# Kernel tuning notes

Measured on AMD Instinct MI355X. Metric: run time of the kernel, lower is better.

The kernel has to match this reference:

```python
import jax, jax.numpy as jnp
import numpy as np

B, N, DIM = 64, 197, 768
H = 12
IN_DIM = 768
HD = IN_DIM // H  # 64


def setup_inputs() -> dict:
    key = jax.random.key(0)
    k1, k2, k3 = jax.random.split(key, 3)
    x = jax.random.normal(k1, (B, N, DIM), dtype=jnp.float32)
    # learnable per-head scale, initialized to head_dim**-0.5
    scale = (DIM // H) ** (-0.5) * jnp.ones((H,), dtype=jnp.float32)
    w_qkv = jax.random.normal(k2, (3 * IN_DIM, DIM), dtype=jnp.float32) * 0.02  # qkv_bias=False
    w_proj = jax.random.normal(k3, (IN_DIM, IN_DIM), dtype=jnp.float32) * 0.02
    b_proj = jnp.zeros((IN_DIM,), dtype=jnp.float32)
    return {"x": x, "scale": scale, "w_qkv": w_qkv, "w_proj": w_proj, "b_proj": b_proj}


def reference(x, scale, w_qkv, w_proj, b_proj):
    Bx, Nx, C = x.shape
    # qkv projection -> [3, B, H, N, HD]
    qkv = jnp.einsum('bnc,oc->bno', x, w_qkv).reshape(Bx, Nx, 3, H, HD)
    qkv = qkv.transpose(2, 0, 3, 1, 4)
    q, k, v = qkv[0], qkv[1], qkv[2]
    # per-head learnable scale (LMSA)
    attn = jnp.einsum('bhid,bhjd->bhij', q, k) * scale[None, :, None, None]
    # diagonal mask -> -inf (self-token masking)
    diag = jnp.eye(Nx, dtype=bool)  # [N, N]
    attn = jnp.where(diag[None, None, :, :], -jnp.inf, attn)
    attn = jax.nn.softmax(attn, axis=-1)
    out = jnp.einsum('bhij,bhjd->bhid', attn, v)  # [B, H, N, HD]
    out = out.transpose(0, 2, 1, 3).reshape(Bx, Nx, IN_DIM)
    out = out @ w_proj.T + b_proj
    return out + x  # num_heads > 1 branch: residual add
```

## Files before the change

kernel.cpp:

```cpp
#include <hip/hip_runtime.h>
#include <cstdint>
#include <cstddef>

#define DEV static __device__ __forceinline__

typedef __attribute__((ext_vector_type(8))) short bf16x8;
typedef __attribute__((ext_vector_type(4))) float f32x4;

constexpr int NB   = 64;
constexpr int NTOK = 197;
constexpr int DIMC = 768;
constexpr int NH   = 12;
constexpr int HDIM = 64;
constexpr int MTOK = NB * NTOK;
constexpr int QKVO = 3 * DIMC;
constexpr int BH   = NB * NH;
constexpr int KROWS = 198;
constexpr int VTS   = 232;
constexpr int OBS   = 68;
constexpr int GM64  = MTOK / 64;

constexpr int BM2  = 256;
constexpr int BN2  = 256;
constexpr int GM2  = (MTOK + BM2 - 1) / BM2;
constexpr int GN2  = QKVO / BN2;
constexpr int NKT  = DIMC / 64;
constexpr int BUFH = 32768;

DEV unsigned short f2bf(float f) {
  union { float f; uint32_t u; } v; v.f = f;
  uint32_t u = v.u;
  return (unsigned short)((u + 0x7FFFu + ((u >> 16) & 1u)) >> 16);
}

DEV uint32_t pack_bf2(float a, float b) {
  return (uint32_t)f2bf(a) | ((uint32_t)f2bf(b) << 16);
}

DEV f32x4 mfma16(bf16x8 a, bf16x8 b, f32x4 c) {
  return __builtin_amdgcn_mfma_f32_16x16x32_bf16(a, b, c, 0, 0, 0);
}

DEV void async_cp16(const unsigned short* g, unsigned short* l) {
  __builtin_amdgcn_global_load_lds(
      (__attribute__((address_space(1))) void*)g,
      (__attribute__((address_space(3))) void*)l, 16, 0, 0);
}

DEV void swizzle_idx(int lin, int gridM, int gridN, int& mt, int& nt) {
  int per = 16 * gridN;
  int sup = lin / per;
  int bm  = sup * 16;
  int Gm  = gridM - bm; if (Gm > 16) Gm = 16;
  int rem = lin - sup * per;
  nt = rem / Gm;
  mt = bm + (rem - nt * Gm);
}

constexpr int CVB1 = (MTOK * DIMC) / 4096;
constexpr int CVB2 = (QKVO * DIMC) / 4096;
constexpr int CVB3 = (DIMC * DIMC) / 4096;
constexpr int CVNB = CVB1 + CVB2 + CVB3;

__global__ void __launch_bounds__(256) cvt_all(const float* __restrict__ x,
                                               const float* __restrict__ wq,
                                               const float* __restrict__ wp,
                                               unsigned short* __restrict__ xb,
                                               unsigned short* __restrict__ wqb,
                                               unsigned short* __restrict__ wpb) {
  int blk = blockIdx.x;
  const float* s; unsigned short* d;
  if (blk < CVB1)               { s = x;  d = xb; }
  else if (blk < CVB1 + CVB2)   { s = wq; d = wqb; blk -= CVB1; }
  else                          { s = wp; d = wpb; blk -= CVB1 + CVB2; }
  size_t base = (size_t)blk * 4096 + (size_t)threadIdx.x * 4;
#pragma unroll
  for (int j = 0; j < 4; ++j) {
    size_t i = base + (size_t)j * 1024;
    float4 f = *(const float4*)(s + i);
    ushort4 o;
    o.x = f2bf(f.x); o.y = f2bf(f.y); o.z = f2bf(f.z); o.w = f2bf(f.w);
    *(ushort4*)(d + i) = o;
  }
}

DEV void stage_A_qm(const unsigned short* A, unsigned short* lds,
                    int mbase, int k0, int qm, int tid) {
#pragma unroll
  for (int u = 0; u < 2; ++u) {
    int c = u * 512 + tid;
    int row = c >> 3, cc = c & 7;
    int arow = qm * 64 + (row & 63) + ((row >> 6) << 7);
    int gr = mbase + arow; gr = gr < MTOK ? gr : MTOK - 1;
    int gc = (cc ^ (arow & 7)) * 8;
    async_cp16(A + (size_t)gr * DIMC + k0 + gc, lds + arow * 64 + cc * 8);
  }
}

DEV void stage_B_qn(const unsigned short* Bw, unsigned short* lds,
                    int nbase, int k0, int qn, int tid) {
#pragma unroll
  for (int u = 0; u < 2; ++u) {
    int c = u * 512 + tid;
    int row = c >> 3, cc = c & 7;
    int brow = (row >> 5) * 64 + qn * 32 + (row & 31);
    int gc = (cc ^ (brow & 7)) * 8;
    async_cp16(Bw + (size_t)(nbase + brow) * DIMC + k0 + gc, lds + brow * 64 + cc * 8);
  }
}

template <int QM>
DEV void ldA(const unsigned short* Ac, int wm, int l16, int quad, bf16x8 (&af)[4][2]) {
#pragma unroll
  for (int mi = 0; mi < 4; ++mi)
#pragma unroll
    for (int kk = 0; kk < 2; ++kk) {
      int r = wm * 128 + QM * 64 + mi * 16 + l16;
      af[mi][kk] = *(const bf16x8*)(Ac + r * 64 + (((kk * 4 + quad) ^ (r & 7)) * 8));
    }
}

template <int QN>
DEV void ldB(const unsigned short* Bc, int wn, int l16, int quad, bf16x8 (&bf_)[2][2]) {
#pragma unroll
  for (int ni = 0; ni < 2; ++ni)
#pragma unroll
    for (int kk = 0; kk < 2; ++kk) {
      int r = wn * 64 + QN * 32 + ni * 16 + l16;
      bf_[ni][kk] = *(const bf16x8*)(Bc + r * 64 + (((kk * 4 + quad) ^ (r & 7)) * 8));
    }
}

template <int QM, int QN>
DEV void ph_mfma(bf16x8 (&af)[4][2], bf16x8 (&bf_)[2][2], f32x4 (&acc)[8][4]) {
  __builtin_amdgcn_s_setprio(1);
#pragma unroll
  for (int kk = 0; kk < 2; ++kk)
#pragma unroll
    for (int mi = 0; mi < 4; ++mi)
#pragma unroll
      for (int ni = 0; ni < 2; ++ni)
        acc[QM * 4 + mi][QN * 2 + ni] =
            mfma16(af[mi][kk], bf_[ni][kk], acc[QM * 4 + mi][QN * 2 + ni]);
  __builtin_amdgcn_s_setprio(0);
}

__global__ void __launch_bounds__(512, 2) gemm_qkv(const unsigned short* __restrict__ A,
                                                   const unsigned short* __restrict__ Bw,
                                                   unsigned short* __restrict__ qkv) {
  extern __shared__ unsigned short lds[];
  const int tid = threadIdx.x, lane = tid & 63, wave = tid >> 6;
  const int wm = wave & 1, wn = wave >> 1;
  const int l16 = lane & 15, quad = lane >> 4;
  int mt, nt;
  swizzle_idx(blockIdx.x, GM2, GN2, mt, nt);
  const int mbase = mt * BM2, nbase = nt * BN2;

  f32x4 acc[8][4];
#pragma unroll
  for (int i = 0; i < 8; ++i)
#pragma unroll
    for (int j = 0; j < 4; ++j) acc[i][j] = {0.f, 0.f, 0.f, 0.f};

  unsigned short* A0 = lds;
  unsigned short* B0 = lds + 16384;
  unsigned short* A1 = lds + BUFH;
  unsigned short* B1 = lds + BUFH + 16384;

  stage_A_qm(A, A0, mbase, 0, 0, tid);
  stage_B_qn(Bw, B0, nbase, 0, 0, tid);
  stage_A_qm(A, A0, mbase, 0, 1, tid);
  stage_B_qn(Bw, B0, nbase, 0, 1, tid);
  stage_A_qm(A, A1, mbase, 64, 0, tid);
  stage_B_qn(Bw, B1, nbase, 64, 0, tid);
  asm volatile("s_waitcnt vmcnt(4)" ::: "memory");
  __builtin_amdgcn_s_barrier();

  bf16x8 af[4][2], b0[2][2], b1[2][2];

  for (int kt = 0; kt < NKT; ++kt) {
    unsigned short* Ac = (kt & 1) ? A1 : A0;
    unsigned short* Bc = (kt & 1) ? B1 : B0;
    unsigned short* An = (kt & 1) ? A0 : A1;
    unsigned short* Bn = (kt & 1) ? B0 : B1;

    ldA<0>(Ac, wm, l16, quad, af);
    ldB<0>(Bc, wn, l16, quad, b0);
    if (kt < NKT - 1) stage_A_qm(A, An, mbase, (kt + 1) * 64, 1, tid);
    __builtin_amdgcn_s_barrier();
    ph_mfma<0, 0>(af, b0, acc);
    asm volatile("s_waitcnt lgkmcnt(0)" ::: "memory");
    __builtin_amdgcn_s_barrier();

    ldB<1>(Bc, wn, l16, quad, b1);
    if (kt < NKT - 1) stage_B_qn(Bw, Bn, nbase, (kt + 1) * 64, 1, tid);
    __builtin_amdgcn_s_barrier();
    ph_mfma<0, 1>(af, b1, acc);
    asm volatile("s_waitcnt lgkmcnt(0)" ::: "memory");
    __builtin_amdgcn_s_barrier();

    ldA<1>(Ac, wm, l16, quad, af);
    if (kt < NKT - 2) stage_A_qm(A, Ac, mbase, (kt + 2) * 64, 0, tid);
    __builtin_amdgcn_s_barrier();
    ph_mfma<1, 0>(af, b0, acc);
    asm volatile("s_waitcnt lgkmcnt(0)" ::: "memory");
    __builtin_amdgcn_s_barrier();

    if (kt < NKT - 2) stage_B_qn(Bw, Bc, nbase, (kt + 2) * 64, 0, tid);
    __builtin_amdgcn_s_barrier();
    ph_mfma<1, 1>(af, b1, acc);
    if (kt >= NKT - 2) asm volatile("s_waitcnt vmcnt(0) lgkmcnt(0)" ::: "memory");
    else               asm volatile("s_waitcnt vmcnt(4) lgkmcnt(0)" ::: "memory");
    __builtin_amdgcn_s_barrier();
  }

  const int oc64  = nbase + wn * 64;
  const int which = oc64 / DIMC;
  const int h     = (oc64 % DIMC) / HDIM;
#pragma unroll
  for (int mi8 = 0; mi8 < 8; ++mi8) {
    int t0 = mbase + wm * 128 + mi8 * 16 + quad * 4;
#pragma unroll
    for (int r = 0; r < 4; ++r) {
      int t = t0 + r;
      if (t < MTOK) {
        int b = t / NTOK, n = t - b * NTOK;
        size_t base = ((size_t)((which * NB + b) * NH + h) * NTOK + n) * HDIM;
#pragma unroll
        for (int ni = 0; ni < 4; ++ni)
          qkv[base + ni * 16 + l16] = f2bf(acc[mi8][ni][r]);
      }
    }
  }
}

__global__ void __launch_bounds__(256) gemm_proj(const unsigned short* __restrict__ A,
                                                 const unsigned short* __restrict__ Bw,
                                                 const float* __restrict__ bias,
                                                 const float* __restrict__ xres,
                                                 float* __restrict__ out) {
  __shared__ __align__(16) unsigned short As[64 * 64];
  __shared__ __align__(16) unsigned short Bs[128 * 64];
  const int tid = threadIdx.x, lane = tid & 63, wave = tid >> 6;
  const int wm = wave & 1, wn = wave >> 1;
  const int l16 = lane & 15, quad = lane >> 4;
  int mt, nt;
  swizzle_idx(blockIdx.x, GM64, DIMC / 128, mt, nt);
  const int mbase = mt * 64, nbase = nt * 128;

  f32x4 acc[2][4];
#pragma unroll
  for (int i = 0; i < 2; ++i)
#pragma unroll
    for (int j = 0; j < 4; ++j) acc[i][j] = {0.f, 0.f, 0.f, 0.f};

  for (int k0 = 0; k0 < DIMC; k0 += 64) {
#pragma unroll
    for (int i = 0; i < 2; ++i) {
      int c = i * 256 + tid;
      int row = c >> 3, cc = c & 7;
      int gc = (cc ^ (row & 7)) * 8;
      async_cp16(A + (size_t)(mbase + row) * DIMC + k0 + gc, As + c * 8);
    }
#pragma unroll
    for (int i = 0; i < 4; ++i) {
      int c = i * 256 + tid;
      int row = c >> 3, cc = c & 7;
      int gc = (cc ^ (row & 7)) * 8;
      async_cp16(Bw + (size_t)(nbase + row) * DIMC + k0 + gc, Bs + c * 8);
    }
    __syncthreads();
#pragma unroll
    for (int kk = 0; kk < 64; kk += 32) {
      const int cw = (kk >> 3) + quad;
      bf16x8 af[2], bfr[4];
#pragma unroll
      for (int mi = 0; mi < 2; ++mi) {
        int r = wm * 32 + mi * 16 + l16;
        af[mi] = *(const bf16x8*)(As + r * 64 + (cw ^ (r & 7)) * 8);
      }
#pragma unroll
      for (int ni = 0; ni < 4; ++ni) {
        int r = wn * 64 + ni * 16 + l16;
        bfr[ni] = *(const bf16x8*)(Bs + r * 64 + (cw ^ (r & 7)) * 8);
      }
#pragma unroll
      for (int mi = 0; mi < 2; ++mi)
#pragma unroll
        for (int ni = 0; ni < 4; ++ni)
          acc[mi][ni] = mfma16(af[mi], bfr[ni], acc[mi][ni]);
    }
    __syncthreads();
  }

  const int oc = nbase + wn * 64;
#pragma unroll
  for (int mi = 0; mi < 2; ++mi) {
    int t0 = mbase + wm * 32 + mi * 16 + quad * 4;
#pragma unroll
    for (int r = 0; r < 4; ++r) {
      int t = t0 + r;
      size_t rowb = (size_t)t * DIMC;
#pragma unroll
      for (int ni = 0; ni < 4; ++ni) {
        int o = oc + ni * 16 + l16;
        out[rowb + o] = acc[mi][ni][r] + bias[o] + xres[rowb + o];
      }
    }
  }
}

__global__ void __launch_bounds__(256, 2) attn_fused(const unsigned short* __restrict__ qkv,
                                                     const float* __restrict__ scale,
                                                     unsigned short* __restrict__ aout) {
  __shared__ __align__(16) unsigned short Ks[KROWS * 64];
  __shared__ __align__(16) unsigned short Vt[HDIM * VTS];
  __shared__ __align__(16) unsigned short Ob[4 * 16 * OBS];

  const int tid = threadIdx.x, lane = tid & 63, wave = tid >> 6;
  const int l16 = lane & 15, quad = lane >> 4;
  const int bh = blockIdx.x;
  const int b = bh / NH, h = bh - b * NH;

  const unsigned short* qg = qkv + (size_t)bh * (NTOK * HDIM);
  const unsigned short* kg = qkv + (size_t)(BH + bh) * (NTOK * HDIM);
  const unsigned short* vg = qkv + (size_t)(2 * BH + bh) * (NTOK * HDIM);
  const float sc = scale[h];

#pragma unroll
  for (int i = 0; i < 7; ++i) {
    int c = i * 256 + tid;
    if (c < KROWS * 8) {
      int row = c >> 3, cc = c & 7;
      async_cp16(kg + (size_t)row * 64 + ((cc ^ (row & 7)) * 8), Ks + c * 8);
    }
  }
  {
    const int dcol = tid & 63;
    const int slab = tid >> 6;
#pragma unroll
    for (int p = 0; p < 7; ++p) {
      int n0 = p * 32 + slab * 8;
      union { unsigned short us[8]; bf16x8 v; } tr;
#pragma unroll
      for (int i = 0; i < 8; ++i) {
        int n = n0 + i; n = n > NTOK - 1 ? NTOK - 1 : n;
        tr.us[i] = vg[(size_t)n * HDIM + dcol];
      }
      *(bf16x8*)(Vt + dcol * VTS + n0) = tr.v;
    }
  }
  __syncthreads();

  const int srcA  = l16 + ((quad & 1) << 5);
  const int srcB  = srcA + 16;
  const int stsel = quad >> 1;
  unsigned short* ob = Ob + wave * (16 * OBS);

  for (int mt = wave; mt < 13; mt += 4) {
    int qr = mt * 16 + l16; if (qr > NTOK - 1) qr = NTOK - 1;
    bf16x8 qb0 = *(const bf16x8*)(qg + (size_t)qr * 64 + quad * 8);
    bf16x8 qb1 = *(const bf16x8*)(qg + (size_t)qr * 64 + 32 + quad * 8);
    const int mg = mt * 16 + l16;

    f32x4 s[7][2];
#pragma unroll
    for (int jc = 0; jc < 7; ++jc)
#pragma unroll
      for (int st = 0; st < 2; ++st) {
        if (jc == 6 && st == 1) { s[6][1] = {0.f, 0.f, 0.f, 0.f}; continue; }
        int jrow = (jc * 2 + st) * 16 + l16;
        jrow = jrow > NTOK ? NTOK : jrow;
        const unsigned short* kr = Ks + jrow * 64;
        bf16x8 ka0 = *(const bf16x8*)(kr + (quad       ^ (jrow & 7)) * 8);
        bf16x8 ka1 = *(const bf16x8*)(kr + ((4 + quad) ^ (jrow & 7)) * 8);
        f32x4 t = {0.f, 0.f, 0.f, 0.f};
        t = mfma16(ka0, qb0, t);
        t = mfma16(ka1, qb1, t);
        s[jc][st] = t;
      }

    float cmax = -1e30f;
#pragma unroll
    for (int jc = 0; jc < 7; ++jc)
#pragma unroll
      for (int st = 0; st < 2; ++st)
#pragma unroll
        for (int r = 0; r < 4; ++r) {
          int jg = jc * 32 + st * 16 + quad * 4 + r;
          float v = s[jc][st][r] * sc;
          v = (jg >= NTOK || jg == mg) ? -1e30f : v;
          s[jc][st][r] = v;
          cmax = fmaxf(cmax, v);
        }
    cmax = fmaxf(cmax, __shfl_xor(cmax, 16));
    cmax = fmaxf(cmax, __shfl_xor(cmax, 32));
    float psum = 0.f;
#pragma unroll
    for (int jc = 0; jc < 7; ++jc)
#pragma unroll
      for (int st = 0; st < 2; ++st)
#pragma unroll
        for (int r = 0; r < 4; ++r) {
          float e = __expf(s[jc][st][r] - cmax);
          psum += e;
          s[jc][st][r] = e;
        }
    psum += __shfl_xor(psum, 16);
    psum += __shfl_xor(psum, 32);
    const float inv = 1.0f / psum;

    f32x4 oacc[4];
#pragma unroll
    for (int dt = 0; dt < 4; ++dt) oacc[dt] = {0.f, 0.f, 0.f, 0.f};

#pragma unroll
    for (int jc = 0; jc < 7; ++jc) {
      uint32_t u0 = pack_bf2(s[jc][0][0], s[jc][0][1]);
      uint32_t v0 = pack_bf2(s[jc][0][2], s[jc][0][3]);
      uint32_t u1 = pack_bf2(s[jc][1][0], s[jc][1][1]);
      uint32_t v1 = pack_bf2(s[jc][1][2], s[jc][1][3]);
      uint32_t au0 = (uint32_t)__shfl((int)u0, srcA);
      uint32_t av0 = (uint32_t)__shfl((int)v0, srcA);
      uint32_t au1 = (uint32_t)__shfl((int)u1, srcA);
      uint32_t av1 = (uint32_t)__shfl((int)v1, srcA);
      uint32_t bu0 = (uint32_t)__shfl((int)u0, srcB);
      uint32_t bv0 = (uint32_t)__shfl((int)v0, srcB);
      uint32_t bu1 = (uint32_t)__shfl((int)u1, srcB);
      uint32_t bv1 = (uint32_t)__shfl((int)v1, srcB);
      union { uint32_t u[4]; bf16x8 v; } pb;
      pb.u[0] = stsel ? au1 : au0;
      pb.u[1] = stsel ? av1 : av0;
      pb.u[2] = stsel ? bu1 : bu0;
      pb.u[3] = stsel ? bv1 : bv0;
#pragma unroll
      for (int dt = 0; dt < 4; ++dt) {
        bf16x8 va = *(const bf16x8*)(Vt + (dt * 16 + l16) * VTS +
                                     jc * 32 + quad * 8);
        oacc[dt] = mfma16(va, pb.v, oacc[dt]);
      }
    }

#pragma unroll
    for (int dt = 0; dt < 4; ++dt) {
      ushort4 pk;
      pk.x = f2bf(oacc[dt][0] * inv);
      pk.y = f2bf(oacc[dt][1] * inv);
      pk.z = f2bf(oacc[dt][2] * inv);
      pk.w = f2bf(oacc[dt][3] * inv);
      *(ushort4*)(ob + l16 * OBS + dt * 16 + quad * 4) = pk;
    }
    __asm__ __volatile__("s_waitcnt lgkmcnt(0)" ::: "memory");
#pragma unroll
    for (int rnd = 0; rnd < 4; ++rnd) {
      int q   = rnd * 4 + (lane >> 4);
      int o8  = lane & 15;
      uint2 d8 = *(const uint2*)(ob + q * OBS + o8 * 4);
      int qrow = mt * 16 + q;
      if (qrow < NTOK) {
        size_t obase = (size_t)(b * NTOK + qrow) * DIMC + h * HDIM;
        *(uint2*)(aout + obase + o8 * 4) = d8;
      }
    }
  }
}

extern "C" void kernel_launch(void* const* d_in, const int* in_sizes, int n_in,
                              void* d_out, int out_size, void* d_ws, size_t ws_size,
                              hipStream_t stream) {
  const float* x     = (const float*)d_in[0];
  const float* scale = (const float*)d_in[1];
  const float* wqkv  = (const float*)d_in[2];
  const float* wproj = (const float*)d_in[3];
  const float* bproj = (const float*)d_in[4];
  float* out = (float*)d_out;

  unsigned short* xb   = (unsigned short*)d_ws;
  unsigned short* wqb  = xb  + (size_t)MTOK * DIMC;
  unsigned short* wpb  = wqb + (size_t)QKVO * DIMC;
  unsigned short* qkvb = wpb + (size_t)DIMC * DIMC;
  unsigned short* attb = xb;

  static bool qkv_attr_set = false;
  if (!qkv_attr_set) {
    hipFuncSetAttribute(reinterpret_cast<const void*>(gemm_qkv),
                        hipFuncAttributeMaxDynamicSharedMemorySize, 131072);
    qkv_attr_set = true;
  }

  cvt_all<<<CVNB, 256, 0, stream>>>(x, wqkv, wproj, xb, wqb, wpb);
  gemm_qkv<<<GM2 * GN2, 512, 131072, stream>>>(xb, wqb, qkvb);
  attn_fused<<<BH, 256, 0, stream>>>(qkvb, scale, attb);
  gemm_proj<<<GM64 * (DIMC / 128), 256, 0, stream>>>(attb, wpb, bproj, x, out);
}
```

Measured before the change: 211.2 us.

## Process two QKV GEMM tiles per block and overlap the first tile's epilogue

The QKV GEMM kernel now launches half as many blocks, and each block computes two output tiles back to back in one continuous double-buffered K pipeline. The epilogue is split into four quadrant stores. The first tile's quadrants are written and their accumulators zeroed right after each MFMA phase at the tile boundary, while loads for the second tile are already in flight. The aim is to hide the first tile's global stores and the prologue fill of the second tile behind ongoing work. In exchange, the grid of 225 blocks may leave some CUs idle, and the hand-tuned vmcnt thresholds must exactly match the new load ordering.

```diff
diff --git a/kernel.cpp b/kernel.cpp
--- a/kernel.cpp
+++ b/kernel.cpp
@@ -25,6 +25,8 @@
 constexpr int GM2  = (MTOK + BM2 - 1) / BM2;
 constexpr int GN2  = QKVO / BN2;
 constexpr int NKT  = DIMC / 64;
+constexpr int TOT  = 2 * NKT;
+constexpr int GRID_QKV = (GM2 * GN2) / 2;
 constexpr int BUFH = 32768;
 
 DEV unsigned short f2bf(float f) {
@@ -145,6 +147,34 @@
   __builtin_amdgcn_s_setprio(0);
 }
 
+template <int QM, int QN>
+DEV void epi_quad(f32x4 (&acc)[8][4], unsigned short* __restrict__ qkv,
+                  int mbase, int nbase, int wm, int wn, int l16, int quad) {
+  const int oc32  = nbase + wn * 64 + QN * 32;
+  const int which = oc32 / DIMC;
+  const int h     = (oc32 % DIMC) / HDIM;
+#pragma unroll
+  for (int mi = 0; mi < 4; ++mi) {
+    int t0 = mbase + wm * 128 + QM * 64 + mi * 16 + quad * 4;
+#pragma unroll
+    for (int r = 0; r < 4; ++r) {
+      int t = t0 + r;
+      if (t < MTOK) {
+        int b = t / NTOK, n = t - b * NTOK;
+        size_t base = ((size_t)((which * NB + b) * NH + h) * NTOK + n) * HDIM;
+#pragma unroll
+        for (int ni = 0; ni < 2; ++ni)
+          qkv[base + QN * 32 + ni * 16 + l16] = f2bf(acc[QM * 4 + mi][QN * 2 + ni][r]);
+      }
+    }
+  }
+#pragma unroll
+  for (int mi = 0; mi < 4; ++mi)
+#pragma unroll
+    for (int ni = 0; ni < 2; ++ni)
+      acc[QM * 4 + mi][QN * 2 + ni] = {0.f, 0.f, 0.f, 0.f};
+}
+
 __global__ void __launch_bounds__(512, 2) gemm_qkv(const unsigned short* __restrict__ A,
                                                    const unsigned short* __restrict__ Bw,
                                                    unsigned short* __restrict__ qkv) {
@@ -152,9 +182,15 @@
   const int tid = threadIdx.x, lane = tid & 63, wave = tid >> 6;
   const int wm = wave & 1, wn = wave >> 1;
   const int l16 = lane & 15, quad = lane >> 4;
-  int mt, nt;
-  swizzle_idx(blockIdx.x, GM2, GN2, mt, nt);
-  const int mbase = mt * BM2, nbase = nt * BN2;
+
+  int mbs[2], nbs[2];
+  {
+    int mt, nt;
+    swizzle_idx(blockIdx.x * 2,     GM2, GN2, mt, nt);
+    mbs[0] = mt * BM2; nbs[0] = nt * BN2;
+    swizzle_idx(blockIdx.x * 2 + 1, GM2, GN2, mt, nt);
+    mbs[1] = mt * BM2; nbs[1] = nt * BN2;
+  }
 
   f32x4 acc[8][4];
 #pragma unroll
@@ -167,71 +203,75 @@
   unsigned short* A1 = lds + BUFH;
   unsigned short* B1 = lds + BUFH + 16384;
 
-  stage_A_qm(A, A0, mbase, 0, 0, tid);
-  stage_B_qn(Bw, B0, nbase, 0, 0, tid);
-  stage_A_qm(A, A0, mbase, 0, 1, tid);
-  stage_B_qn(Bw, B0, nbase, 0, 1, tid);
-  stage_A_qm(A, A1, mbase, 64, 0, tid);
-  stage_B_qn(Bw, B1, nbase, 64, 0, tid);
+  stage_A_qm(A, A0, mbs[0], 0, 0, tid);
+  stage_B_qn(Bw, B0, nbs[0], 0, 0, tid);
+  stage_A_qm(A, A0, mbs[0], 0, 1, tid);
+  stage_B_qn(Bw, B0, nbs[0], 0, 1, tid);
+  stage_A_qm(A, A1, mbs[0], 64, 0, tid);
+  stage_B_qn(Bw, B1, nbs[0], 64, 0, tid);
   asm volatile("s_waitcnt vmcnt(4)" ::: "memory");
   __builtin_amdgcn_s_barrier();
 
   bf16x8 af[4][2], b0[2][2], b1[2][2];
 
-  for (int kt = 0; kt < NKT; ++kt) {
-    unsigned short* Ac = (kt & 1) ? A1 : A0;
-    unsigned short* Bc = (kt & 1) ? B1 : B0;
-    unsigned short* An = (kt & 1) ? A0 : A1;
-    unsigned short* Bn = (kt & 1) ? B0 : B1;
+  for (int ktg = 0; ktg < TOT; ++ktg) {
+    unsigned short* Ac = (ktg & 1) ? A1 : A0;
+    unsigned short* Bc = (ktg & 1) ? B1 : B0;
+    unsigned short* An = (ktg & 1) ? A0 : A1;
+    unsigned short* Bn = (ktg & 1) ? B0 : B1;
 
     ldA<0>(Ac, wm, l16, quad, af);
     ldB<0>(Bc, wn, l16, quad, b0);
-    if (kt < NKT - 1) stage_A_qm(A, An, mbase, (kt + 1) * 64, 1, tid);
+    if (ktg + 1 < TOT) {
+      int tg = ktg + 1, t1 = tg >= NKT;
+      stage_A_qm(A, An, mbs[t1], (tg - t1 * NKT) * 64, 1, tid);
+    }
     __builtin_amdgcn_s_barrier();
     ph_mfma<0, 0>(af, b0, acc);
-    asm volatile("s_waitcnt lgkmcnt(0)" ::: "memory");
-    __builtin_amdgcn_s_barrier();
+    if (ktg < TOT - 1) asm volatile("s_waitcnt vmcnt(6) lgkmcnt(0)" ::: "memory");
+    else               asm volatile("s_waitcnt vmcnt(0) lgkmcnt(0)" ::: "memory");
+    __builtin_amdgcn_s_barrier();
+    if (ktg == NKT - 1) epi_quad<0, 0>(acc, qkv, mbs[0], nbs[0], wm, wn, l16, quad);
 
     ldB<1>(Bc, wn, l16, quad, b1);
-    if (kt < NKT - 1) stage_B_qn(Bw, Bn, nbase, (kt + 1) * 64, 1, tid);
+    if (ktg + 1 < TOT) {
+      int tg = ktg + 1, t1 = tg >= NKT;
+      stage_B_qn(Bw, Bn, nbs[t1], (tg - t1 * NKT) * 64, 1, tid);
+    }
     __builtin_amdgcn_s_barrier();
     ph_mfma<0, 1>(af, b1, acc);
     asm volatile("s_waitcnt lgkmcnt(0)" ::: "memory");
     __builtin_amdgcn_s_barrier();
+    if (ktg == NKT - 1) epi_quad<0, 1>(acc, qkv, mbs[0], nbs[0], wm, wn, l16, quad);
 
     ldA<1>(Ac, wm, l16, quad, af);
-    if (kt < NKT - 2) stage_A_qm(A, Ac, mbase, (kt + 2) * 64, 0, tid);
+    if (ktg + 2 < TOT) {
+      int tg = ktg + 2, t1 = tg >= NKT;
+      stage_A_qm(A, Ac, mbs[t1], (tg - t1 * NKT) * 64, 0, tid);
+    }
     __builtin_amdgcn_s_barrier();
     ph_mfma<1, 0>(af, b0, acc);
     asm volatile("s_waitcnt lgkmcnt(0)" ::: "memory");
     __builtin_amdgcn_s_barrier();
-
-    if (kt < NKT - 2) stage_B_qn(Bw, Bc, nbase, (kt + 2) * 64, 0, tid);
+    if (ktg == NKT - 1) epi_quad<1, 0>(acc, qkv, mbs[0], nbs[0], wm, wn, l16, quad);
+
+    if (ktg + 2 < TOT) {
+      int tg = ktg + 2, t1 = tg >= NKT;
+      stage_B_qn(Bw, Bc, nbs[t1], (tg - t1 * NKT) * 64, 0, tid);
+    }
     __builtin_amdgcn_s_barrier();
     ph_mfma<1, 1>(af, b1, acc);
-    if (kt >= NKT - 2) asm volatile("s_waitcnt vmcnt(0) lgkmcnt(0)" ::: "memory");
-    else               asm volatile("s_waitcnt vmcnt(4) lgkmcnt(0)" ::: "memory");
-    __builtin_amdgcn_s_barrier();
-  }
-
-  const int oc64  = nbase + wn * 64;
-  const int which = oc64 / DIMC;
-  const int h     = (oc64 % DIMC) / HDIM;
-#pragma unroll
-  for (int mi8 = 0; mi8 < 8; ++mi8) {
-    int t0 = mbase + wm * 128 + mi8 * 16 + quad * 4;
-#pragma unroll
-    for (int r = 0; r < 4; ++r) {
-      int t = t0 + r;
-      if (t < MTOK) {
-        int b = t / NTOK, n = t - b * NTOK;
-        size_t base = ((size_t)((which * NB + b) * NH + h) * NTOK + n) * HDIM;
-#pragma unroll
-        for (int ni = 0; ni < 4; ++ni)
-          qkv[base + ni * 16 + l16] = f2bf(acc[mi8][ni][r]);
-      }
-    }
-  }
+    if (ktg < TOT - 2)       asm volatile("s_waitcnt vmcnt(8) lgkmcnt(0)" ::: "memory");
+    else if (ktg == TOT - 2) asm volatile("s_waitcnt vmcnt(4) lgkmcnt(0)" ::: "memory");
+    else                     asm volatile("s_waitcnt vmcnt(0) lgkmcnt(0)" ::: "memory");
+    __builtin_amdgcn_s_barrier();
+    if (ktg == NKT - 1) epi_quad<1, 1>(acc, qkv, mbs[0], nbs[0], wm, wn, l16, quad);
+  }
+
+  epi_quad<0, 0>(acc, qkv, mbs[1], nbs[1], wm, wn, l16, quad);
+  epi_quad<0, 1>(acc, qkv, mbs[1], nbs[1], wm, wn, l16, quad);
+  epi_quad<1, 0>(acc, qkv, mbs[1], nbs[1], wm, wn, l16, quad);
+  epi_quad<1, 1>(acc, qkv, mbs[1], nbs[1], wm, wn, l16, quad);
 }
 
 __global__ void __launch_bounds__(256) gemm_proj(const unsigned short* __restrict__ A,
@@ -489,7 +529,7 @@
   }
 
   cvt_all<<<CVNB, 256, 0, stream>>>(x, wqkv, wproj, xb, wqb, wpb);
-  gemm_qkv<<<GM2 * GN2, 512, 131072, stream>>>(xb, wqb, qkvb);
+  gemm_qkv<<<GRID_QKV, 512, 131072, stream>>>(xb, wqb, qkvb);
   attn_fused<<<BH, 256, 0, stream>>>(qkvb, scale, attb);
   gemm_proj<<<GM64 * (DIMC / 128), 256, 0, stream>>>(attb, wpb, bproj, x, out);
 }
```

New measurement: 233.2 us. 10.4% more time.
